# Kernel tuning notes

Hardware: AMD Instinct MI355X
Metric: run time of the kernel (lower is better)

## Reference

```python
import jax, jax.numpy as jnp
import numpy as np
import math

N, DM, DK, DV, KWIN = 500, 2048, 2048, 2048, 10

def _xavier(key, shape):
    fan_out, fan_in = shape[0], shape[1]
    limit = math.sqrt(6.0 / (fan_in + fan_out))
    return jax.random.uniform(key, (shape[0], shape[1]), jnp.float32, -limit, limit)

def setup_inputs() -> dict:
    key = jax.random.key(0)
    ks = jax.random.split(key, 7)
    X = jax.random.normal(ks[0], (N, DM), jnp.float32)
    mask = jax.random.randint(ks[1], (N, N), 0, 2, jnp.int32)
    # torch Linear weight is (out, in); store transposed so fwd is X @ W
    Wq = _xavier(ks[2], (DK, DM)).T  # [DM, DK]
    Wk = _xavier(ks[3], (DK, DM)).T
    Wv = _xavier(ks[4], (DV, DM)).T
    Wo = _xavier(ks[5], (DM, DV)).T  # [DV, DM]
    wk = _xavier(ks[6], (2 * KWIN + 1, DM))  # relative-position embedding table
    return {"X": X, "mask": mask, "Wq": Wq, "Wk": Wk, "Wv": Wv, "Wo": Wo, "wk": wk}

def reference(X, mask, Wq, Wk, Wv, Wo, wk):
    n = X.shape[0]
    scale = 1.0 / math.sqrt(DK)
    Q = X @ Wq            # [n, dk]
    K = X @ Wk            # [n, dk]
    V = X @ Wv            # [n, dv]
    Qs = Q * scale
    S = Qs @ K.T          # [n, n] content scores
    # relative-position bias: Sr[i,j] = Qs[i] . wk[clip(j-i,-k,k)+k]
    # (Shaw-style gather; identical math to wk[table] matmul, no [n,n,dm] intermediate)
    idx = jnp.clip(jnp.arange(n)[None, :] - jnp.arange(n)[:, None], -KWIN, KWIN) + KWIN  # [n, n]
    QR = Qs @ wk.T                                   # [n, 2k+1]
    Sr = jnp.take_along_axis(QR, idx, axis=1)        # [n, n]
    S = S + Sr
    S = jnp.where(mask == 0, jnp.float32(-1e9), S)
    A = jax.nn.softmax(S, axis=-1)                   # dropout_rate=0 -> identity
    Y = (A @ V) @ Wo                                 # [n, dm]
    return (Y, A)
```

## Files before the change

kernel.cpp:

```cpp
#include <hip/hip_runtime.h>
#include <hip/hip_bf16.h>


#define N_TOK 500
#define MP 512
#define DM 2048
#define KWIN_ 10
#define NREL 21

typedef __hip_bfloat16 bf16;
typedef __attribute__((ext_vector_type(8))) short short8;
typedef __attribute__((ext_vector_type(4))) float floatx4;

#define NS 262144L

__device__ inline float bfj(const short8& v, int j) {
  return __bfloat162float(((const bf16*)&v)[j]);
}

__device__ __forceinline__ void gload16(const bf16* g, bf16* l) {
  __builtin_amdgcn_global_load_lds(
      (const __attribute__((address_space(1))) void*)g,
      (__attribute__((address_space(3))) void*)l, 16, 0, 0);
}

__global__ __launch_bounds__(256) void prep(
    const float* __restrict__ Wq, const float* __restrict__ Wk,
    const float* __restrict__ Wv, const float* __restrict__ Wo,
    const float* __restrict__ X, const float* __restrict__ wk,
    bf16* __restrict__ WqkT, bf16* __restrict__ WvT, bf16* __restrict__ WoT,
    bf16* __restrict__ Xb, bf16* __restrict__ wkb) {
  int z = blockIdx.z;
  int tid = threadIdx.x;
  if (z == 4) {
    int row = blockIdx.y * 32 + blockIdx.x;
    int c0 = tid * 8;
    bf16 v[8];
    if (row < MP) {
      if (row < N_TOK) {
        const float* p = X + (long)row * DM + c0;
#pragma unroll
        for (int j = 0; j < 8; ++j) v[j] = __float2bfloat16(p[j]);
      } else {
#pragma unroll
        for (int j = 0; j < 8; ++j) v[j] = __float2bfloat16(0.f);
      }
      *(short8*)(Xb + (long)row * DM + c0) = *(short8*)v;
    } else if (row < MP + NREL) {
      int r = row - MP;
      const float* p = wk + (long)r * DM + c0;
#pragma unroll
      for (int j = 0; j < 8; ++j) v[j] = __float2bfloat16(p[j]);
      *(short8*)(wkb + (long)r * DM + c0) = *(short8*)v;
    }
    return;
  }
  const float* W = (z == 0) ? Wq : (z == 1) ? Wk : (z == 2) ? Wv : Wo;
  bf16* Out = (z == 0) ? WqkT
            : (z == 1) ? (WqkT + (long)DM * DM)
            : (z == 2) ? WvT : WoT;
  __shared__ float t[64][68];
  int k0 = blockIdx.y * 64, n0 = blockIdx.x * 64;
  int rr = tid >> 4, cc = (tid & 15) * 4;
  int gsw = cc >> 2;
#pragma unroll
  for (int p = 0; p < 4; ++p) {
    int r = rr + 16 * p;
    float4 v = *(const float4*)(W + (long)(k0 + r) * DM + n0 + cc);
    *(float4*)&t[r][(gsw ^ (r & 3)) * 4] = v;
  }
  __syncthreads();
#pragma unroll
  for (int s0 = 0; s0 < 2; ++s0) {
    int s = tid + s0 * 256;
    int n = s >> 3, c = s & 7;
    bf16 v[8];
#pragma unroll
    for (int j = 0; j < 8; ++j) {
      int rowt = c * 8 + j;
      int col = ((n >> 2) ^ (rowt & 3)) * 4 + (n & 3);
      v[j] = __float2bfloat16(t[rowt][col]);
    }
    *(short8*)(Out + (long)(n0 + n) * DM + k0 + c * 8) = *(short8*)v;
  }
}

template <int BM, int OUT>
__device__ __forceinline__ void gemm_core(
    bf16 (*sm)[256][32], const bf16* __restrict__ A, int lda,
    const bf16* __restrict__ B, int ldb, float* __restrict__ Cf,
    bf16* __restrict__ Cb, int ldc, int kStart, int kLen, int row0, int col0,
    int mLim) {
  constexpr int GM = (BM == 128) ? 4 : 2;
  int tid = threadIdx.x;
  int lane = tid & 63, w = tid >> 6;
  int l16 = lane & 15, l4 = lane >> 4;
  int lrow = lane >> 2, lcol = (lane & 3) * 8;
  int wr = (w & 1) * (16 * GM), wc = (w >> 1) * 64;
  const bf16* Ab = A + (long)row0 * lda + kStart;
  const bf16* Bb = B + (long)col0 * ldb + kStart;
  const int arow0 = (BM == 128) ? 32 * w : 16 * w;
  const bf16* aSrc0 = Ab + (long)(arow0 + lrow) * lda + lcol;
  const bf16* aSrc1 = Ab + (long)(arow0 + 16 + lrow) * lda + lcol;
  const bf16* bSrc0 = Bb + (long)(32 * w + lrow) * ldb + lcol;
  const bf16* bSrc1 = Bb + (long)(32 * w + 16 + lrow) * ldb + lcol;

  floatx4 acc[GM][4] = {};

#define STAGE(buf, kk)                                          \
  do {                                                          \
    gload16(aSrc0 + (kk), &sm[buf][arow0][0]);                  \
    if (BM == 128) gload16(aSrc1 + (kk), &sm[buf][arow0 + 16][0]); \
    gload16(bSrc0 + (kk), &sm[buf][128 + 32 * w][0]);           \
    gload16(bSrc1 + (kk), &sm[buf][128 + 32 * w + 16][0]);      \
  } while (0)

  STAGE(0, 0);
  int cur = 0;
  for (int k0 = 0; k0 < kLen; k0 += 32) {
    int kn = k0 + 32;
    if (kn < kLen) {
      STAGE(cur ^ 1, kn);
      if (BM == 128)
        asm volatile("s_waitcnt vmcnt(4)" ::: "memory");
      else
        asm volatile("s_waitcnt vmcnt(3)" ::: "memory");
    } else {
      asm volatile("s_waitcnt vmcnt(0)" ::: "memory");
    }
    __builtin_amdgcn_s_barrier();
    __builtin_amdgcn_sched_barrier(0);
    short8 af[GM], bg[4];
#pragma unroll
    for (int g = 0; g < GM; ++g)
      af[g] = *(const short8*)&sm[cur][wr + g * 16 + l16][l4 * 8];
#pragma unroll
    for (int h = 0; h < 4; ++h)
      bg[h] = *(const short8*)&sm[cur][128 + wc + h * 16 + l16][l4 * 8];
#pragma unroll
    for (int g = 0; g < GM; ++g)
#pragma unroll
      for (int h = 0; h < 4; ++h)
        acc[g][h] = __builtin_amdgcn_mfma_f32_16x16x32_bf16(af[g], bg[h],
                                                            acc[g][h], 0, 0, 0);
    __builtin_amdgcn_sched_barrier(0);
    asm volatile("s_waitcnt lgkmcnt(0)" ::: "memory");
    __builtin_amdgcn_s_barrier();
    cur ^= 1;
  }
#undef STAGE

#pragma unroll
  for (int g = 0; g < GM; ++g)
#pragma unroll
    for (int h = 0; h < 4; ++h)
#pragma unroll
      for (int i = 0; i < 4; ++i) {
        long r = row0 + wr + g * 16 + l4 * 4 + i;
        long c = col0 + wc + h * 16 + l16;
        if (r < mLim) {
          if (OUT == 0)
            Cf[r * ldc + c] = acc[g][h][i];
          else
            Cb[r * ldc + c] = __float2bfloat16(acc[g][h][i]);
        }
      }
}

__global__ __launch_bounds__(256, 2) void gemm_qkvt(
    const bf16* __restrict__ Xb, const bf16* __restrict__ WqkT,
    const bf16* __restrict__ WvT, bf16* __restrict__ QKbf,
    bf16* __restrict__ Vtb) {
  __shared__ __align__(16) bf16 sm[2][256][32];
  int id = blockIdx.x;
  if (id < 128) {
    int row0 = (id >> 5) * 128, col0 = (id & 31) * 128;
    gemm_core<128, 1>(sm, Xb, DM, WqkT, DM, nullptr, QKbf, 4096, 0, DM, row0,
                      col0, MP);
  } else {
    int t = id - 128;
    int row0 = (t >> 2) * 64, col0 = (t & 3) * 128;
    gemm_core<64, 1>(sm, WvT, DM, Xb, DM, nullptr, Vtb, MP, 0, DM, row0, col0,
                     DM);
  }
}

template <int BM, int OUT>
__global__ __launch_bounds__(256, 2) void gemm_k(
    const bf16* __restrict__ A, int lda, const bf16* __restrict__ B, int ldb,
    float* __restrict__ Cf, bf16* __restrict__ Cb, int ldc, int sliceK,
    long cstride, int mLim) {
  __shared__ __align__(16) bf16 sm[2][256][32];
  float* cf = (OUT == 0) ? Cf + (long)blockIdx.z * cstride : nullptr;
  gemm_core<BM, OUT>(sm, A, lda, B, ldb, cf, Cb, ldc, blockIdx.z * sliceK,
                     sliceK, blockIdx.y * BM, blockIdx.x * 128, mLim);
}

__global__ __launch_bounds__(256) void softmax_qr(
    const float* __restrict__ Sp, const bf16* __restrict__ QKbf,
    const bf16* __restrict__ wkb, const int* __restrict__ mask,
    float* __restrict__ Aout, bf16* __restrict__ Abf) {
  int i = blockIdx.x;
  int tid = threadIdx.x;
  if (i >= N_TOK) {
    Abf[(long)i * MP + tid] = __float2bfloat16(0.f);
    Abf[(long)i * MP + tid + 256] = __float2bfloat16(0.f);
    return;
  }
  int lane = tid & 63, w = tid >> 6;
  __shared__ float sQR[24];
  __shared__ float red[4];
  short8 q[4];
#pragma unroll
  for (int s = 0; s < 4; ++s)
    q[s] = *(const short8*)(QKbf + (long)i * 4096 + s * 512 + lane * 8);
  for (int r = w; r < NREL; r += 4) {
    float p = 0.f;
#pragma unroll
    for (int s = 0; s < 4; ++s) {
      short8 wv = *(const short8*)(wkb + (long)r * DM + s * 512 + lane * 8);
#pragma unroll
      for (int j = 0; j < 8; ++j) p += bfj(q[s], j) * bfj(wv, j);
    }
#pragma unroll
    for (int o = 32; o > 0; o >>= 1) p += __shfl_down(p, o);
    if (lane == 0) sQR[r] = p;
  }
  __syncthreads();
  const float scale = 0.022097086912079608f;
  float v0, v1 = -1e30f;
  int j0 = tid, j1 = tid + 256;
  {
    float s = Sp[(long)i * MP + j0] + Sp[NS + (long)i * MP + j0] +
              Sp[2 * NS + (long)i * MP + j0] + Sp[3 * NS + (long)i * MP + j0];
    int rel = j0 - i;
    rel = rel < -KWIN_ ? -KWIN_ : (rel > KWIN_ ? KWIN_ : rel);
    s = scale * (s + sQR[rel + KWIN_]);
    if (mask[(long)i * N_TOK + j0] == 0) s = -1e9f;
    v0 = s;
  }
  if (j1 < N_TOK) {
    float s = Sp[(long)i * MP + j1] + Sp[NS + (long)i * MP + j1] +
              Sp[2 * NS + (long)i * MP + j1] + Sp[3 * NS + (long)i * MP + j1];
    int rel = j1 - i;
    rel = rel < -KWIN_ ? -KWIN_ : (rel > KWIN_ ? KWIN_ : rel);
    s = scale * (s + sQR[rel + KWIN_]);
    if (mask[(long)i * N_TOK + j1] == 0) s = -1e9f;
    v1 = s;
  }
  float mx = fmaxf(v0, v1);
#pragma unroll
  for (int o = 32; o > 0; o >>= 1) mx = fmaxf(mx, __shfl_down(mx, o));
  if (lane == 0) red[w] = mx;
  __syncthreads();
  if (tid == 0) red[0] = fmaxf(fmaxf(red[0], red[1]), fmaxf(red[2], red[3]));
  __syncthreads();
  mx = red[0];
  __syncthreads();
  float e0 = expf(v0 - mx);
  float e1 = (j1 < N_TOK) ? expf(v1 - mx) : 0.f;
  float sum = e0 + e1;
#pragma unroll
  for (int o = 32; o > 0; o >>= 1) sum += __shfl_down(sum, o);
  if (lane == 0) red[w] = sum;
  __syncthreads();
  if (tid == 0) red[0] = red[0] + red[1] + red[2] + red[3];
  __syncthreads();
  float inv = 1.f / red[0];
  float a0 = e0 * inv, a1 = e1 * inv;
  Aout[(long)i * N_TOK + j0] = a0;
  if (j1 < N_TOK) Aout[(long)i * N_TOK + j1] = a1;
  Abf[(long)i * MP + j0] = __float2bfloat16(a0);
  Abf[(long)i * MP + j1] = __float2bfloat16(a1);
}

extern "C" void kernel_launch(void* const* d_in, const int* in_sizes, int n_in,
                              void* d_out, int out_size, void* d_ws,
                              size_t ws_size, hipStream_t stream) {
  const float* X = (const float*)d_in[0];
  const int* mask = (const int*)d_in[1];
  const float* Wq = (const float*)d_in[2];
  const float* Wk = (const float*)d_in[3];
  const float* Wv = (const float*)d_in[4];
  const float* Wo = (const float*)d_in[5];
  const float* wk = (const float*)d_in[6];

  float* Yout = (float*)d_out;
  float* Aout = Yout + (long)N_TOK * DM;

  const long MB = 1 << 20;
  char* p = (char*)d_ws;
  bf16* Xb = (bf16*)p;
  bf16* WqkT = (bf16*)(p + 2 * MB);
  bf16* WvT = (bf16*)(p + 18 * MB);
  bf16* WoT = (bf16*)(p + 26 * MB);
  bf16* wkb = (bf16*)(p + 34 * MB);
  bf16* QKbf = (bf16*)(p + 35 * MB);
  bf16* Vtb = (bf16*)(p + 39 * MB);
  float* Sp = (float*)(p + 41 * MB);
  bf16* Abf = (bf16*)(p + 45 * MB);
  bf16* AVbf = (bf16*)(p + 46 * MB);

  dim3 b256(256);

  prep<<<dim3(32, 32, 5), b256, 0, stream>>>(Wq, Wk, Wv, Wo, X, wk, WqkT, WvT,
                                             WoT, Xb, wkb);
  gemm_qkvt<<<dim3(256), b256, 0, stream>>>(Xb, WqkT, WvT, QKbf, Vtb);
  gemm_k<64, 0><<<dim3(4, 8, 4), b256, 0, stream>>>(
      QKbf, 4096, QKbf + 2048, 4096, Sp, nullptr, MP, 512, NS, MP);
  softmax_qr<<<dim3(MP), b256, 0, stream>>>(Sp, QKbf, wkb, mask, Aout, Abf);
  gemm_k<64, 1><<<dim3(16, 8, 1), b256, 0, stream>>>(
      Abf, MP, Vtb, MP, nullptr, AVbf, DM, MP, 0, MP);
  gemm_k<64, 0><<<dim3(16, 8, 1), b256, 0, stream>>>(
      AVbf, DM, WoT, DM, Yout, nullptr, DM, DM, 0, N_TOK);
}
```

Before: 189.4 us.

## Deepen GEMM LDS pipeline to four stages, swizzle LDS, double split-K for scores

The shared GEMM core moves from double buffering to a four-buffer ring with three tiles in flight, so more global-to-LDS loads are outstanding while MFMAs run. LDS columns are XOR-swizzled on both write and read to cut bank conflicts. The QK^T score GEMM goes from split-K 4 to split-K 8, giving 256 blocks instead of 128, and softmax now sums 8 partials. The cost is twice the LDS per block, which may limit occupancy, plus extra partial-sum traffic. Workspace offsets are shifted to make room for the larger partial buffer.

```diff
diff --git a/kernel.cpp b/kernel.cpp
--- a/kernel.cpp
+++ b/kernel.cpp
@@ -87,56 +87,63 @@
 
 template <int BM, int OUT>
 __device__ __forceinline__ void gemm_core(
-    bf16 (*sm)[256][32], const bf16* __restrict__ A, int lda,
-    const bf16* __restrict__ B, int ldb, float* __restrict__ Cf,
-    bf16* __restrict__ Cb, int ldc, int kStart, int kLen, int row0, int col0,
-    int mLim) {
+    bf16* sm, const bf16* __restrict__ A, int lda, const bf16* __restrict__ B,
+    int ldb, float* __restrict__ Cf, bf16* __restrict__ Cb, int ldc,
+    int kStart, int kLen, int row0, int col0, int mLim) {
   constexpr int GM = (BM == 128) ? 4 : 2;
+  constexpr int ROWS = BM + 128;
+  constexpr int BUFE = ROWS * 32;
   int tid = threadIdx.x;
   int lane = tid & 63, w = tid >> 6;
   int l16 = lane & 15, l4 = lane >> 4;
-  int lrow = lane >> 2, lcol = (lane & 3) * 8;
+  int lrow = lane >> 2;
+  int lcol = ((lane & 3) ^ ((lane >> 3) & 3)) * 8;
   int wr = (w & 1) * (16 * GM), wc = (w >> 1) * 64;
   const bf16* Ab = A + (long)row0 * lda + kStart;
   const bf16* Bb = B + (long)col0 * ldb + kStart;
   const int arow0 = (BM == 128) ? 32 * w : 16 * w;
+  const int brow0 = BM + 32 * w;
   const bf16* aSrc0 = Ab + (long)(arow0 + lrow) * lda + lcol;
   const bf16* aSrc1 = Ab + (long)(arow0 + 16 + lrow) * lda + lcol;
   const bf16* bSrc0 = Bb + (long)(32 * w + lrow) * ldb + lcol;
   const bf16* bSrc1 = Bb + (long)(32 * w + 16 + lrow) * ldb + lcol;
 
   floatx4 acc[GM][4] = {};
-
-#define STAGE(buf, kk)                                          \
-  do {                                                          \
-    gload16(aSrc0 + (kk), &sm[buf][arow0][0]);                  \
-    if (BM == 128) gload16(aSrc1 + (kk), &sm[buf][arow0 + 16][0]); \
-    gload16(bSrc0 + (kk), &sm[buf][128 + 32 * w][0]);           \
-    gload16(bSrc1 + (kk), &sm[buf][128 + 32 * w + 16][0]);      \
+  int NT = kLen >> 5;
+
+#define STAGE(buf, kk)                                                \
+  do {                                                                \
+    bf16* bp = sm + (buf) * BUFE;                                     \
+    gload16(aSrc0 + (kk), bp + arow0 * 32);                           \
+    if (BM == 128) gload16(aSrc1 + (kk), bp + (arow0 + 16) * 32);     \
+    gload16(bSrc0 + (kk), bp + brow0 * 32);                           \
+    gload16(bSrc1 + (kk), bp + (brow0 + 16) * 32);                    \
   } while (0)
 
   STAGE(0, 0);
-  int cur = 0;
-  for (int k0 = 0; k0 < kLen; k0 += 32) {
-    int kn = k0 + 32;
-    if (kn < kLen) {
-      STAGE(cur ^ 1, kn);
+  STAGE(1, 32);
+  STAGE(2, 64);
+  int rd = ((l16 >> 1) & 3) * 8;
+  for (int t = 0; t < NT; ++t) {
+    if (t + 3 < NT) {
+      STAGE((t + 3) & 3, (t + 3) * 32);
       if (BM == 128)
-        asm volatile("s_waitcnt vmcnt(4)" ::: "memory");
+        asm volatile("s_waitcnt vmcnt(12)" ::: "memory");
       else
-        asm volatile("s_waitcnt vmcnt(3)" ::: "memory");
+        asm volatile("s_waitcnt vmcnt(9)" ::: "memory");
     } else {
       asm volatile("s_waitcnt vmcnt(0)" ::: "memory");
     }
     __builtin_amdgcn_s_barrier();
     __builtin_amdgcn_sched_barrier(0);
+    const bf16* bp = sm + (t & 3) * BUFE;
     short8 af[GM], bg[4];
 #pragma unroll
     for (int g = 0; g < GM; ++g)
-      af[g] = *(const short8*)&sm[cur][wr + g * 16 + l16][l4 * 8];
+      af[g] = *(const short8*)(bp + (wr + g * 16 + l16) * 32 + (l4 * 8 ^ rd));
 #pragma unroll
     for (int h = 0; h < 4; ++h)
-      bg[h] = *(const short8*)&sm[cur][128 + wc + h * 16 + l16][l4 * 8];
+      bg[h] = *(const short8*)(bp + (BM + wc + h * 16 + l16) * 32 + (l4 * 8 ^ rd));
 #pragma unroll
     for (int g = 0; g < GM; ++g)
 #pragma unroll
@@ -146,7 +153,6 @@
     __builtin_amdgcn_sched_barrier(0);
     asm volatile("s_waitcnt lgkmcnt(0)" ::: "memory");
     __builtin_amdgcn_s_barrier();
-    cur ^= 1;
   }
 #undef STAGE
 
@@ -171,7 +177,7 @@
     const bf16* __restrict__ Xb, const bf16* __restrict__ WqkT,
     const bf16* __restrict__ WvT, bf16* __restrict__ QKbf,
     bf16* __restrict__ Vtb) {
-  __shared__ __align__(16) bf16 sm[2][256][32];
+  __shared__ __align__(16) bf16 sm[4 * 256 * 32];
   int id = blockIdx.x;
   if (id < 128) {
     int row0 = (id >> 5) * 128, col0 = (id & 31) * 128;
@@ -190,7 +196,7 @@
     const bf16* __restrict__ A, int lda, const bf16* __restrict__ B, int ldb,
     float* __restrict__ Cf, bf16* __restrict__ Cb, int ldc, int sliceK,
     long cstride, int mLim) {
-  __shared__ __align__(16) bf16 sm[2][256][32];
+  __shared__ __align__(16) bf16 sm[4 * (BM + 128) * 32];
   float* cf = (OUT == 0) ? Cf + (long)blockIdx.z * cstride : nullptr;
   gemm_core<BM, OUT>(sm, A, lda, B, ldb, cf, Cb, ldc, blockIdx.z * sliceK,
                      sliceK, blockIdx.y * BM, blockIdx.x * 128, mLim);
@@ -231,8 +237,9 @@
   float v0, v1 = -1e30f;
   int j0 = tid, j1 = tid + 256;
   {
-    float s = Sp[(long)i * MP + j0] + Sp[NS + (long)i * MP + j0] +
-              Sp[2 * NS + (long)i * MP + j0] + Sp[3 * NS + (long)i * MP + j0];
+    float s = 0.f;
+#pragma unroll
+    for (int z = 0; z < 8; ++z) s += Sp[z * NS + (long)i * MP + j0];
     int rel = j0 - i;
     rel = rel < -KWIN_ ? -KWIN_ : (rel > KWIN_ ? KWIN_ : rel);
     s = scale * (s + sQR[rel + KWIN_]);
@@ -240,8 +247,9 @@
     v0 = s;
   }
   if (j1 < N_TOK) {
-    float s = Sp[(long)i * MP + j1] + Sp[NS + (long)i * MP + j1] +
-              Sp[2 * NS + (long)i * MP + j1] + Sp[3 * NS + (long)i * MP + j1];
+    float s = 0.f;
+#pragma unroll
+    for (int z = 0; z < 8; ++z) s += Sp[z * NS + (long)i * MP + j1];
     int rel = j1 - i;
     rel = rel < -KWIN_ ? -KWIN_ : (rel > KWIN_ ? KWIN_ : rel);
     s = scale * (s + sQR[rel + KWIN_]);
@@ -298,16 +306,16 @@
   bf16* QKbf = (bf16*)(p + 35 * MB);
   bf16* Vtb = (bf16*)(p + 39 * MB);
   float* Sp = (float*)(p + 41 * MB);
-  bf16* Abf = (bf16*)(p + 45 * MB);
-  bf16* AVbf = (bf16*)(p + 46 * MB);
+  bf16* Abf = (bf16*)(p + 49 * MB);
+  bf16* AVbf = (bf16*)(p + 50 * MB);
 
   dim3 b256(256);
 
   prep<<<dim3(32, 32, 5), b256, 0, stream>>>(Wq, Wk, Wv, Wo, X, wk, WqkT, WvT,
                                              WoT, Xb, wkb);
   gemm_qkvt<<<dim3(256), b256, 0, stream>>>(Xb, WqkT, WvT, QKbf, Vtb);
-  gemm_k<64, 0><<<dim3(4, 8, 4), b256, 0, stream>>>(
-      QKbf, 4096, QKbf + 2048, 4096, Sp, nullptr, MP, 512, NS, MP);
+  gemm_k<64, 0><<<dim3(4, 8, 8), b256, 0, stream>>>(
+      QKbf, 4096, QKbf + 2048, 4096, Sp, nullptr, MP, 256, NS, MP);
   softmax_qr<<<dim3(MP), b256, 0, stream>>>(Sp, QKbf, wkb, mask, Aout, Abf);
   gemm_k<64, 1><<<dim3(16, 8, 1), b256, 0, stream>>>(
       Abf, MP, Vtb, MP, nullptr, AVbf, DM, MP, 0, MP);
```

After: 178.8 us. 5.6% less time.
